# Kernel optimization log

Measured on AMD Instinct MI355X. Metric: run time of the kernel, lower is better.

## Reference

```python
import jax, jax.numpy as jnp
import numpy as np

B, S, D, F, E, DT, K = 4, 2048, 1024, 4096, 8, 256, 2


def setup_inputs() -> dict:
    key = jax.random.key(0)
    ks = jax.random.split(key, 8)
    scale_g = 1.0 / np.sqrt(D)
    scale_t = 1.0 / np.sqrt(DT)
    scale_1 = 1.0 / np.sqrt(D)
    scale_2 = 1.0 / np.sqrt(F)
    return {
        "inputs": jax.random.normal(ks[0], (B, S, D), dtype=jnp.float32),
        "task_param": jax.random.normal(ks[1], (B, 1, DT), dtype=jnp.float32),
        "Wg_in": jax.random.normal(ks[2], (D, E), dtype=jnp.float32) * scale_g,
        "bg_in": jnp.zeros((E,), dtype=jnp.float32),
        "Wg_task": jax.random.normal(ks[3], (DT, E), dtype=jnp.float32) * scale_t,
        "bg_task": jnp.zeros((E,), dtype=jnp.float32),
        "alpha": jnp.float32(0.5),
        "W1": jax.random.normal(ks[4], (E, D, F), dtype=jnp.float32) * scale_1,
        "b1": jnp.zeros((E, F), dtype=jnp.float32),
        "W2": jax.random.normal(ks[5], (E, F, D), dtype=jnp.float32) * scale_2,
        "b2": jnp.zeros((E, D), dtype=jnp.float32),
    }


def reference(inputs, task_param, Wg_in, bg_in, Wg_task, bg_task, alpha, W1, b1, W2, b2):
    # Gating: blend input-gate and task-gate logits ([B,1,E] broadcasts over S)
    input_logits = jnp.einsum('bsd,de->bse', inputs, Wg_in) + bg_in
    task_logits = jnp.einsum('btd,de->bte', task_param, Wg_task) + bg_task
    gate_logits = (1.0 - alpha) * input_logits + alpha * task_logits  # [B,S,E]

    topk_vals, selected = jax.lax.top_k(gate_logits, K)  # [B,S,K]

    # Load-balancing auxiliary loss (float32 softmax, as in the original)
    weights_softmax = jax.nn.softmax(gate_logits.astype(jnp.float32), axis=-1).astype(inputs.dtype)
    average_weight = jnp.mean(weights_softmax, axis=(0, 1))  # [E]
    onehot = jax.nn.one_hot(selected, E, dtype=inputs.dtype)  # [B,S,K,E]
    average_count = jnp.mean(onehot.sum(axis=2), axis=(0, 1))  # [E]
    l_aux = jnp.mean(average_weight * average_count) * E

    # Combine weights: softmax over the top-k gate values
    w = jax.nn.softmax(topk_vals.astype(jnp.float32), axis=-1).astype(inputs.dtype)  # [B,S,K]

    # Dense expert compute (same math as the per-expert gather/scatter loop)
    h = jax.nn.silu(jnp.einsum('bsd,edf->ebsf', inputs, W1) + b1[:, None, None, :])  # [E,B,S,F]
    expert_out = jnp.einsum('ebsf,efd->ebsd', h, W2) + b2[:, None, None, :]          # [E,B,S,D]

    picked = jnp.einsum('bske,ebsd->bskd', onehot, expert_out)  # [B,S,K,D]
    results = jnp.einsum('bsk,bskd->bsd', w, picked)            # [B,S,D]
    return results, l_aux.astype(jnp.float32)
```

## Files before the change

kernel.cpp:

```cpp
#include <hip/hip_runtime.h>

#define T_TOK 8192
#define D_DIM 1024
#define F_DIM 4096
#define E_EXP 8
#define DT_DIM 256
#define GBLK 256

#define A_XB   0u
#define A_WT   16777216u
#define A_H    83886080u
#define A_Y    226492416u
#define A_META 262144000u
#define MO_FILL   0
#define MO_PB     64
#define MO_NT     128
#define MO_PARTP  256
#define MO_PARTC  8448
#define MO_TILEE  16640
#define MO_TILERB 17664
#define MO_ROUTEE 18688
#define MO_ROUTEW 84224
#define MO_TSLOT  149760
#define MO_PTOK   215296
#define META_BYTES 284928
#define META_INTS  (META_BYTES/4)

using bf16x8 = __attribute__((ext_vector_type(8))) short;
using f32x4  = __attribute__((ext_vector_type(4))) float;
typedef unsigned short u16;

__device__ __forceinline__ u16 f2bf(float f) {
  union { float f; unsigned u; } v; v.f = f;
  unsigned r = v.u + 0x7FFFu + ((v.u >> 16) & 1u);
  return (u16)(r >> 16);
}
__device__ __forceinline__ float bf2f(u16 h) {
  union { unsigned u; float f; } v; v.u = ((unsigned)h) << 16; return v.f;
}
__device__ __forceinline__ void gload16(const void* gsrc, void* ldst) {
  __builtin_amdgcn_global_load_lds(
      (const __attribute__((address_space(1))) void*)gsrc,
      (__attribute__((address_space(3))) void*)ldst, 16, 0, 0);
}

__global__ void zerok(int* p, int n) {
  int i = blockIdx.x * 256 + threadIdx.x;
  if (i < n) p[i] = 0;
}

__global__ __launch_bounds__(256) void tcvt(const float* __restrict__ src,
                                            u16* __restrict__ dst, int R, int C) {
  __shared__ u16 tile[32][33];
  size_t off = (size_t)blockIdx.z * R * C;
  int cb = blockIdx.x * 32, rb = blockIdx.y * 32;
  int tx = threadIdx.x & 31, ty = threadIdx.x >> 5;
#pragma unroll
  for (int i = 0; i < 4; i++)
    tile[ty + i * 8][tx] = f2bf(src[off + (size_t)(rb + ty + i * 8) * C + cb + tx]);
  __syncthreads();
#pragma unroll
  for (int i = 0; i < 4; i++)
    dst[off + (size_t)(cb + ty + i * 8) * R + rb + tx] = tile[tx][ty + i * 8];
}

__global__ __launch_bounds__(256) void gating(
    const float* __restrict__ X, const float* __restrict__ TP,
    const float* __restrict__ Wg, const float* __restrict__ bg,
    const float* __restrict__ Wt, const float* __restrict__ bgt,
    const float* __restrict__ alphaP, u16* __restrict__ Xb, int* meta) {
  __shared__ float WgT[E_EXP * D_DIM];
  __shared__ float WtT[E_EXP * DT_DIM];
  __shared__ float wsP[4][8];
  __shared__ int   wsC[4][8];
  int tid = threadIdx.x;
  for (int i = tid; i < E_EXP * D_DIM; i += 256) { int d = i >> 3, e = i & 7; WgT[e * D_DIM + d] = Wg[i]; }
  for (int i = tid; i < E_EXP * DT_DIM; i += 256) { int d = i >> 3, e = i & 7; WtT[e * DT_DIM + d] = Wt[i]; }
  __syncthreads();
  int lane = tid & 63, wid = tid >> 6;
  int tb = blockIdx.x * 32;
  int b = tb >> 11;
  float alpha = alphaP[0];

  float tac[8] = {};
#pragma unroll
  for (int i = 0; i < 4; i++) {
    int d = lane + i * 64;
    float x = TP[b * DT_DIM + d];
#pragma unroll
    for (int e = 0; e < 8; e++) tac[e] += x * WtT[e * DT_DIM + d];
  }
  for (int off = 32; off > 0; off >>= 1)
#pragma unroll
    for (int e = 0; e < 8; e++) tac[e] += __shfl_xor(tac[e], off);
  float tl[8];
#pragma unroll
  for (int e = 0; e < 8; e++) tl[e] = alpha * (tac[e] + bgt[e]);

  float psum[8] = {};
  int   cnt[8] = {};
  for (int i = 0; i < 8; i++) {
    int t = tb + wid * 8 + i;
    const float* xr = X + (size_t)t * D_DIM;
    float acc[8] = {};
    u16 xb[16];
#pragma unroll 4
    for (int j = 0; j < 16; j++) {
      int d = lane + j * 64;
      float x = xr[d];
      xb[j] = f2bf(x);
#pragma unroll
      for (int e = 0; e < 8; e++) acc[e] += x * WgT[e * D_DIM + d];
    }
#pragma unroll
    for (int j = 0; j < 16; j++) Xb[(size_t)t * D_DIM + lane + j * 64] = xb[j];
    for (int off = 32; off > 0; off >>= 1)
#pragma unroll
      for (int e = 0; e < 8; e++) acc[e] += __shfl_xor(acc[e], off);
    float gl[8];
#pragma unroll
    for (int e = 0; e < 8; e++) gl[e] = (1.f - alpha) * (acc[e] + bg[e]) + tl[e];
    int e1 = 0;
#pragma unroll
    for (int e = 1; e < 8; e++) if (gl[e] > gl[e1]) e1 = e;
    int es = (e1 == 0) ? 1 : 0;
#pragma unroll
    for (int e = 0; e < 8; e++) if (e != e1 && gl[e] > gl[es]) es = e;
    float mx = gl[0];
#pragma unroll
    for (int e = 1; e < 8; e++) mx = fmaxf(mx, gl[e]);
    float pe[8], se = 0.f;
#pragma unroll
    for (int e = 0; e < 8; e++) { pe[e] = __expf(gl[e] - mx); se += pe[e]; }
    float inv = 1.f / se;
    if (lane == 0) {
#pragma unroll
      for (int e = 0; e < 8; e++) psum[e] += pe[e] * inv;
      cnt[e1]++; cnt[es]++;
      float w1 = 1.f / (1.f + __expf(gl[es] - gl[e1]));
      meta[MO_ROUTEE / 4 + 2 * t] = e1;
      meta[MO_ROUTEE / 4 + 2 * t + 1] = es;
      ((float*)meta)[MO_ROUTEW / 4 + 2 * t] = w1;
      ((float*)meta)[MO_ROUTEW / 4 + 2 * t + 1] = 1.f - w1;
    }
  }
  if (lane == 0) {
#pragma unroll
    for (int e = 0; e < 8; e++) { wsP[wid][e] = psum[e]; wsC[wid][e] = cnt[e]; }
  }
  __syncthreads();
  if (tid < 8) {
    float p = wsP[0][tid] + wsP[1][tid] + wsP[2][tid] + wsP[3][tid];
    int   c = wsC[0][tid] + wsC[1][tid] + wsC[2][tid] + wsC[3][tid];
    ((float*)meta)[MO_PARTP / 4 + blockIdx.x * 8 + tid] = p;
    meta[MO_PARTC / 4 + blockIdx.x * 8 + tid] = c;
  }
}

__global__ void plan(int* meta, float* out) {
  __shared__ float sp[8];
  __shared__ int   sc[8];
  int tid = threadIdx.x;
  if (blockIdx.x != 0) return;
  if (tid < 8) {
    const float* pp = (const float*)meta + MO_PARTP / 4;
    const int*   pc = meta + MO_PARTC / 4;
    float p = 0.f; int c = 0;
    for (int b = 0; b < GBLK; b++) { p += pp[b * 8 + tid]; c += pc[b * 8 + tid]; }
    sp[tid] = p; sc[tid] = c;
  }
  __syncthreads();
  if (tid == 0) {
    int* pb = meta + MO_PB / 4;
    int* tileE = meta + MO_TILEE / 4;
    int* tileRB = meta + MO_TILERB / 4;
    int base = 0, nt = 0;
    float la = 0.f;
    for (int e = 0; e < 8; e++) {
      int n = sc[e];
      pb[e] = base;
      int ntl = (n + 127) >> 7;
      for (int i = 0; i < ntl; i++) { tileE[nt] = e; tileRB[nt] = base + (i << 7); nt++; }
      base += ntl << 7;
      la += (sp[e] * (1.f / 8192.f)) * ((float)n * (1.f / 8192.f));
    }
    pb[8] = base;
    meta[MO_NT / 4] = nt;
    out[T_TOK * D_DIM] = la;
  }
}

__global__ __launch_bounds__(256) void fillk(int* meta) {
  int t = blockIdx.x * 256 + threadIdx.x;
  int lane = threadIdx.x & 63;
  int* pb = meta + MO_PB / 4;
  int* fl = meta + MO_FILL / 4;
  int* ptok = meta + MO_PTOK / 4;
  int* ts = meta + MO_TSLOT / 4;
  unsigned long long lmask = (1ull << lane) - 1;
#pragma unroll
  for (int k = 0; k < 2; k++) {
    int e = meta[MO_ROUTEE / 4 + 2 * t + k];
    int slot = 0;
    for (int ee = 0; ee < 8; ee++) {
      unsigned long long mask = __ballot(e == ee);
      if (e == ee) {
        int low = __ffsll((long long)mask) - 1;
        int pre = __popcll(mask & lmask);
        int base = 0;
        if (lane == low) base = atomicAdd(&fl[ee], __popcll(mask));
        base = __shfl(base, low);
        slot = pb[ee] + base + pre;
      }
    }
    ptok[slot] = t;
    ts[2 * t + k] = slot;
  }
}


__global__ __launch_bounds__(256) void gemm1(
    const u16* __restrict__ Xb, const u16* __restrict__ W1T,
    const float* __restrict__ b1, u16* __restrict__ H, const int* __restrict__ meta) {
  int nt = meta[MO_NT / 4];
  int bt = blockIdx.x;
  if (bt >= nt) return;
  int e = meta[MO_TILEE / 4 + bt];
  int rb = meta[MO_TILERB / 4 + bt];
  int cb = blockIdx.y * 128;
  const int* ptok = meta + MO_PTOK / 4;

  __shared__ short sA[128 * 64];
  __shared__ short sB[128 * 64];
  int tid = threadIdx.x, lane = tid & 63, wid = tid >> 6;
  int wr = wid >> 1, wc = wid & 1;

  int gsrc = ((lane & 7) ^ (lane >> 3)) * 8;
  const u16* srcA[4];
  const u16* srcB[4];
#pragma unroll
  for (int c = 0; c < 4; c++) {
    int rr = c * 32 + wid * 8 + (lane >> 3);
    int tok = ptok[rb + rr];
    srcA[c] = Xb + (size_t)tok * D_DIM + gsrc;
    srcB[c] = W1T + ((size_t)e * F_DIM + cb + rr) * D_DIM + gsrc;
  }

  f32x4 acc[4][4] = {};
  int g0 = lane >> 4, swz = lane & 7;
  int ra = wr * 64 + (lane & 15);
  int rn = wc * 64 + (lane & 15);
  for (int k0 = 0; k0 < D_DIM; k0 += 64) {
    __syncthreads();
#pragma unroll
    for (int c = 0; c < 4; c++) {
      gload16(srcA[c] + k0, (char*)sA + c * 4096 + wid * 1024);
      gload16(srcB[c] + k0, (char*)sB + c * 4096 + wid * 1024);
    }
    __syncthreads();
#pragma unroll
    for (int kk = 0; kk < 2; kk++) {
      bf16x8 af[4], bf[4];
      int gg = ((kk * 4 + g0) ^ swz) * 8;
#pragma unroll
      for (int m = 0; m < 4; m++)
        af[m] = *(const bf16x8*)(sA + (ra + m * 16) * 64 + gg);
#pragma unroll
      for (int n = 0; n < 4; n++)
        bf[n] = *(const bf16x8*)(sB + (rn + n * 16) * 64 + gg);
#pragma unroll
      for (int m = 0; m < 4; m++)
#pragma unroll
        for (int n = 0; n < 4; n++)
          acc[m][n] = __builtin_amdgcn_mfma_f32_16x16x32_bf16(af[m], bf[n], acc[m][n], 0, 0, 0);
    }
  }
  int rbase = wr * 64 + ((lane >> 4) << 2);
  int cbase = cb + wc * 64 + (lane & 15);
#pragma unroll
  for (int m = 0; m < 4; m++)
#pragma unroll
    for (int n = 0; n < 4; n++) {
      int f = cbase + n * 16;
      float bias = b1[e * F_DIM + f];
#pragma unroll
      for (int r = 0; r < 4; r++) {
        int p = rb + rbase + m * 16 + r;
        float v = acc[m][n][r] + bias;
        float s = v * (1.0f / (1.0f + __expf(-v)));
        H[(size_t)p * F_DIM + f] = f2bf(s);
      }
    }
}

__global__ __launch_bounds__(256) void gemm2(
    const u16* __restrict__ H, const u16* __restrict__ W2T,
    const float* __restrict__ b2, u16* __restrict__ Y, const int* __restrict__ meta) {
  int nt = meta[MO_NT / 4];
  int bt = blockIdx.y;
  if (bt >= nt) return;
  int e = meta[MO_TILEE / 4 + bt];
  int rb = meta[MO_TILERB / 4 + bt];
  int cb = blockIdx.x * 128;

  __shared__ short sA[128 * 64];
  __shared__ short sB[128 * 64];
  int tid = threadIdx.x, lane = tid & 63, wid = tid >> 6;
  int wr = wid >> 1, wc = wid & 1;

  int gsrc = ((lane & 7) ^ (lane >> 3)) * 8;
  const u16* srcA[4];
  const u16* srcB[4];
#pragma unroll
  for (int c = 0; c < 4; c++) {
    int rr = c * 32 + wid * 8 + (lane >> 3);
    srcA[c] = H + (size_t)(rb + rr) * F_DIM + gsrc;
    srcB[c] = W2T + ((size_t)e * D_DIM + cb + rr) * F_DIM + gsrc;
  }

  f32x4 acc[4][4] = {};
  int g0 = lane >> 4, swz = lane & 7;
  int ra = wr * 64 + (lane & 15);
  int rn = wc * 64 + (lane & 15);
  for (int k0 = 0; k0 < F_DIM; k0 += 64) {
    __syncthreads();
#pragma unroll
    for (int c = 0; c < 4; c++) {
      gload16(srcA[c] + k0, (char*)sA + c * 4096 + wid * 1024);
      gload16(srcB[c] + k0, (char*)sB + c * 4096 + wid * 1024);
    }
    __syncthreads();
#pragma unroll
    for (int kk = 0; kk < 2; kk++) {
      bf16x8 af[4], bf[4];
      int gg = ((kk * 4 + g0) ^ swz) * 8;
#pragma unroll
      for (int m = 0; m < 4; m++)
        af[m] = *(const bf16x8*)(sA + (ra + m * 16) * 64 + gg);
#pragma unroll
      for (int n = 0; n < 4; n++)
        bf[n] = *(const bf16x8*)(sB + (rn + n * 16) * 64 + gg);
#pragma unroll
      for (int m = 0; m < 4; m++)
#pragma unroll
        for (int n = 0; n < 4; n++)
          acc[m][n] = __builtin_amdgcn_mfma_f32_16x16x32_bf16(af[m], bf[n], acc[m][n], 0, 0, 0);
    }
  }
  int rbase = wr * 64 + ((lane >> 4) << 2);
  int cbase = cb + wc * 64 + (lane & 15);
#pragma unroll
  for (int m = 0; m < 4; m++)
#pragma unroll
    for (int n = 0; n < 4; n++) {
      int d = cbase + n * 16;
      float bias = b2[e * D_DIM + d];
#pragma unroll
      for (int r = 0; r < 4; r++) {
        int p = rb + rbase + m * 16 + r;
        Y[(size_t)p * D_DIM + d] = f2bf(acc[m][n][r] + bias);
      }
    }
}

__global__ __launch_bounds__(256) void combine(const u16* __restrict__ Y,
                                               const int* __restrict__ meta,
                                               float* __restrict__ out) {
  int t = blockIdx.x;
  const int* ts = meta + MO_TSLOT / 4;
  const float* rw = (const float*)meta + MO_ROUTEW / 4;
  int s1 = ts[2 * t], s2 = ts[2 * t + 1];
  float w1 = rw[2 * t], w2 = rw[2 * t + 1];
  int d0 = threadIdx.x * 4;
  ushort4 a = *(const ushort4*)(Y + (size_t)s1 * D_DIM + d0);
  ushort4 b = *(const ushort4*)(Y + (size_t)s2 * D_DIM + d0);
  float4 v;
  v.x = w1 * bf2f(a.x) + w2 * bf2f(b.x);
  v.y = w1 * bf2f(a.y) + w2 * bf2f(b.y);
  v.z = w1 * bf2f(a.z) + w2 * bf2f(b.z);
  v.w = w1 * bf2f(a.w) + w2 * bf2f(b.w);
  *(float4*)(out + (size_t)t * D_DIM + d0) = v;
}

extern "C" void kernel_launch(void* const* d_in, const int* in_sizes, int n_in,
                              void* d_out, int out_size, void* d_ws, size_t ws_size,
                              hipStream_t stream) {
  (void)in_sizes; (void)n_in; (void)out_size; (void)ws_size;
  const float* X    = (const float*)d_in[0];
  const float* TP   = (const float*)d_in[1];
  const float* Wg   = (const float*)d_in[2];
  const float* bg   = (const float*)d_in[3];
  const float* Wt   = (const float*)d_in[4];
  const float* bgt  = (const float*)d_in[5];
  const float* alp  = (const float*)d_in[6];
  const float* W1   = (const float*)d_in[7];
  const float* b1   = (const float*)d_in[8];
  const float* W2   = (const float*)d_in[9];
  const float* b2   = (const float*)d_in[10];
  float* out = (float*)d_out;
  char* ws = (char*)d_ws;
  u16* Xb = (u16*)(ws + A_XB);
  u16* WT = (u16*)(ws + A_WT);
  u16* H  = (u16*)(ws + A_H);
  u16* Y  = (u16*)(ws + A_Y);
  int* meta = (int*)(ws + A_META);

  zerok<<<(META_INTS + 255) / 256, 256, 0, stream>>>(meta, META_INTS);
  tcvt<<<dim3(F_DIM / 32, D_DIM / 32, E_EXP), 256, 0, stream>>>(W1, WT, D_DIM, F_DIM);
  gating<<<GBLK, 256, 0, stream>>>(X, TP, Wg, bg, Wt, bgt, alp, Xb, meta);
  plan<<<1, 64, 0, stream>>>(meta, out);
  fillk<<<T_TOK / 256, 256, 0, stream>>>(meta);
  gemm1<<<dim3(136, F_DIM / 128), 256, 0, stream>>>(Xb, WT, b1, H, meta);
  tcvt<<<dim3(D_DIM / 32, F_DIM / 32, E_EXP), 256, 0, stream>>>(W2, WT, F_DIM, D_DIM);
  gemm2<<<dim3(8, 136), 256, 0, stream>>>(H, WT, b2, Y, meta);
  combine<<<T_TOK, 256, 0, stream>>>(Y, meta, out);
}
```

Baseline: 660.3 us.

## Double-buffer LDS tiles in expert GEMMs and remap blocks for XCD locality

Both grouped GEMMs now use two LDS buffers and prefetch the next K-slice with async global-to-LDS loads while MFMAs run on the current one. Partial vmcnt waits and raised wave priority during compute replace the two syncthreads per step. The grid is flattened to 1D, with a remap that spreads consecutive block ids across the 8 XCDs so blocks sharing a tile land together and reuse L2. LDS use per block doubles to 64 KB, with launch bounds requesting 2 blocks per CU.

After: 664.6 us. No clear change (+0.7%).

```diff
diff --git a/kernel.cpp b/kernel.cpp
--- a/kernel.cpp
+++ b/kernel.cpp
@@ -219,19 +219,21 @@
 }
 
 
-__global__ __launch_bounds__(256) void gemm1(
+__global__ __launch_bounds__(256, 2) void gemm1(
     const u16* __restrict__ Xb, const u16* __restrict__ W1T,
     const float* __restrict__ b1, u16* __restrict__ H, const int* __restrict__ meta) {
+  int id = blockIdx.x;
+  int wg = (id & 7) * 544 + (id >> 3);
+  int bt = wg % 136;
+  int cb = (wg / 136) * 128;
   int nt = meta[MO_NT / 4];
-  int bt = blockIdx.x;
   if (bt >= nt) return;
   int e = meta[MO_TILEE / 4 + bt];
   int rb = meta[MO_TILERB / 4 + bt];
-  int cb = blockIdx.y * 128;
   const int* ptok = meta + MO_PTOK / 4;
 
-  __shared__ short sA[128 * 64];
-  __shared__ short sB[128 * 64];
+  __shared__ short sA[2][128 * 64];
+  __shared__ short sB[2][128 * 64];
   int tid = threadIdx.x, lane = tid & 63, wid = tid >> 6;
   int wr = wid >> 1, wc = wid & 1;
 
@@ -250,30 +252,45 @@
   int g0 = lane >> 4, swz = lane & 7;
   int ra = wr * 64 + (lane & 15);
   int rn = wc * 64 + (lane & 15);
+
+#define STAGE1(buf, k0)                                                  \
+  _Pragma("unroll") for (int c = 0; c < 4; c++) {                        \
+    gload16(srcA[c] + (k0), (char*)&sA[buf][0] + c * 4096 + wid * 1024); \
+    gload16(srcB[c] + (k0), (char*)&sB[buf][0] + c * 4096 + wid * 1024); \
+  }
+
+  STAGE1(0, 0);
+  int cur = 0;
   for (int k0 = 0; k0 < D_DIM; k0 += 64) {
-    __syncthreads();
-#pragma unroll
-    for (int c = 0; c < 4; c++) {
-      gload16(srcA[c] + k0, (char*)sA + c * 4096 + wid * 1024);
-      gload16(srcB[c] + k0, (char*)sB + c * 4096 + wid * 1024);
-    }
-    __syncthreads();
+    if (k0 + 64 < D_DIM) {
+      STAGE1(cur ^ 1, k0 + 64);
+      asm volatile("s_waitcnt vmcnt(8)" ::: "memory");
+    } else {
+      asm volatile("s_waitcnt vmcnt(0)" ::: "memory");
+    }
+    __builtin_amdgcn_s_barrier();
+    __builtin_amdgcn_s_setprio(1);
+    const short* pA = &sA[cur][0];
+    const short* pB = &sB[cur][0];
 #pragma unroll
     for (int kk = 0; kk < 2; kk++) {
       bf16x8 af[4], bf[4];
       int gg = ((kk * 4 + g0) ^ swz) * 8;
 #pragma unroll
       for (int m = 0; m < 4; m++)
-        af[m] = *(const bf16x8*)(sA + (ra + m * 16) * 64 + gg);
+        af[m] = *(const bf16x8*)(pA + (ra + m * 16) * 64 + gg);
 #pragma unroll
       for (int n = 0; n < 4; n++)
-        bf[n] = *(const bf16x8*)(sB + (rn + n * 16) * 64 + gg);
+        bf[n] = *(const bf16x8*)(pB + (rn + n * 16) * 64 + gg);
 #pragma unroll
       for (int m = 0; m < 4; m++)
 #pragma unroll
         for (int n = 0; n < 4; n++)
           acc[m][n] = __builtin_amdgcn_mfma_f32_16x16x32_bf16(af[m], bf[n], acc[m][n], 0, 0, 0);
     }
+    __builtin_amdgcn_s_setprio(0);
+    __builtin_amdgcn_s_barrier();
+    cur ^= 1;
   }
   int rbase = wr * 64 + ((lane >> 4) << 2);
   int cbase = cb + wc * 64 + (lane & 15);
@@ -293,18 +310,20 @@
     }
 }
 
-__global__ __launch_bounds__(256) void gemm2(
+__global__ __launch_bounds__(256, 2) void gemm2(
     const u16* __restrict__ H, const u16* __restrict__ W2T,
     const float* __restrict__ b2, u16* __restrict__ Y, const int* __restrict__ meta) {
+  int id = blockIdx.x;
+  int wg = (id & 7) * 136 + (id >> 3);
+  int bt = wg >> 3;
+  int cb = (wg & 7) * 128;
   int nt = meta[MO_NT / 4];
-  int bt = blockIdx.y;
   if (bt >= nt) return;
   int e = meta[MO_TILEE / 4 + bt];
   int rb = meta[MO_TILERB / 4 + bt];
-  int cb = blockIdx.x * 128;
-
-  __shared__ short sA[128 * 64];
-  __shared__ short sB[128 * 64];
+
+  __shared__ short sA[2][128 * 64];
+  __shared__ short sB[2][128 * 64];
   int tid = threadIdx.x, lane = tid & 63, wid = tid >> 6;
   int wr = wid >> 1, wc = wid & 1;
 
@@ -322,30 +341,45 @@
   int g0 = lane >> 4, swz = lane & 7;
   int ra = wr * 64 + (lane & 15);
   int rn = wc * 64 + (lane & 15);
+
+#define STAGE2(buf, k0)                                                  \
+  _Pragma("unroll") for (int c = 0; c < 4; c++) {                        \
+    gload16(srcA[c] + (k0), (char*)&sA[buf][0] + c * 4096 + wid * 1024); \
+    gload16(srcB[c] + (k0), (char*)&sB[buf][0] + c * 4096 + wid * 1024); \
+  }
+
+  STAGE2(0, 0);
+  int cur = 0;
   for (int k0 = 0; k0 < F_DIM; k0 += 64) {
-    __syncthreads();
-#pragma unroll
-    for (int c = 0; c < 4; c++) {
-      gload16(srcA[c] + k0, (char*)sA + c * 4096 + wid * 1024);
-      gload16(srcB[c] + k0, (char*)sB + c * 4096 + wid * 1024);
-    }
-    __syncthreads();
+    if (k0 + 64 < F_DIM) {
+      STAGE2(cur ^ 1, k0 + 64);
+      asm volatile("s_waitcnt vmcnt(8)" ::: "memory");
+    } else {
+      asm volatile("s_waitcnt vmcnt(0)" ::: "memory");
+    }
+    __builtin_amdgcn_s_barrier();
+    __builtin_amdgcn_s_setprio(1);
+    const short* pA = &sA[cur][0];
+    const short* pB = &sB[cur][0];
 #pragma unroll
     for (int kk = 0; kk < 2; kk++) {
       bf16x8 af[4], bf[4];
       int gg = ((kk * 4 + g0) ^ swz) * 8;
 #pragma unroll
       for (int m = 0; m < 4; m++)
-        af[m] = *(const bf16x8*)(sA + (ra + m * 16) * 64 + gg);
+        af[m] = *(const bf16x8*)(pA + (ra + m * 16) * 64 + gg);
 #pragma unroll
       for (int n = 0; n < 4; n++)
-        bf[n] = *(const bf16x8*)(sB + (rn + n * 16) * 64 + gg);
+        bf[n] = *(const bf16x8*)(pB + (rn + n * 16) * 64 + gg);
 #pragma unroll
       for (int m = 0; m < 4; m++)
 #pragma unroll
         for (int n = 0; n < 4; n++)
           acc[m][n] = __builtin_amdgcn_mfma_f32_16x16x32_bf16(af[m], bf[n], acc[m][n], 0, 0, 0);
     }
+    __builtin_amdgcn_s_setprio(0);
+    __builtin_amdgcn_s_barrier();
+    cur ^= 1;
   }
   int rbase = wr * 64 + ((lane >> 4) << 2);
   int cbase = cb + wc * 64 + (lane & 15);
@@ -410,8 +444,8 @@
   gating<<<GBLK, 256, 0, stream>>>(X, TP, Wg, bg, Wt, bgt, alp, Xb, meta);
   plan<<<1, 64, 0, stream>>>(meta, out);
   fillk<<<T_TOK / 256, 256, 0, stream>>>(meta);
-  gemm1<<<dim3(136, F_DIM / 128), 256, 0, stream>>>(Xb, WT, b1, H, meta);
+  gemm1<<<4352, 256, 0, stream>>>(Xb, WT, b1, H, meta);
   tcvt<<<dim3(D_DIM / 32, F_DIM / 32, E_EXP), 256, 0, stream>>>(W2, WT, F_DIM, D_DIM);
-  gemm2<<<dim3(8, 136), 256, 0, stream>>>(H, WT, b2, Y, meta);
+  gemm2<<<1088, 256, 0, stream>>>(H, WT, b2, Y, meta);
   combine<<<T_TOK, 256, 0, stream>>>(Y, meta, out);
 }
```

## Enlarge grouped GEMM tiles to 256x256 with double-buffered LDS pipeline

Applied to the files above, without the earlier changes.

Both expert GEMMs move from 128x128 tiles with 256 threads to 256x256 tiles with 512 threads. Global-to-LDS loads are double-buffered so the next K-slice is fetched while the current one runs on MFMA. The block index is remapped for XCD-aware scheduling, the routing plan now emits 256-row tiles over 128-padded segments, and stores are guarded by a per-expert row end. Larger tiles raise arithmetic intensity and cut redundant weight traffic, but the last tile of each expert wastes more work and register and LDS pressure goes up.

New measurement: 740.1 us. +12.1%, slower.

```diff
diff --git a/kernel.cpp b/kernel.cpp
--- a/kernel.cpp
+++ b/kernel.cpp
@@ -179,9 +179,10 @@
     for (int e = 0; e < 8; e++) {
       int n = sc[e];
       pb[e] = base;
-      int ntl = (n + 127) >> 7;
-      for (int i = 0; i < ntl; i++) { tileE[nt] = e; tileRB[nt] = base + (i << 7); nt++; }
-      base += ntl << 7;
+      int seg = ((n + 127) >> 7) << 7;
+      int ntl = (seg + 255) >> 8;
+      for (int i = 0; i < ntl; i++) { tileE[nt] = e; tileRB[nt] = base + (i << 8); nt++; }
+      base += seg;
       la += (sp[e] * (1.f / 8192.f)) * ((float)n * (1.f / 8192.f));
     }
     pb[8] = base;
@@ -219,146 +220,135 @@
 }
 
 
-__global__ __launch_bounds__(256) void gemm1(
+#define GEMM_PRE(KDIM)                                                        \
+  __shared__ short sA[2][256 * 64];                                           \
+  __shared__ short sB[2][256 * 64];                                           \
+  int tid = threadIdx.x, lane = tid & 63, wid = tid >> 6;                     \
+  int wr = wid >> 2, wc = wid & 3;                                            \
+  int sw8 = ((tid & 7) ^ ((tid >> 3) & 7)) * 8;                               \
+  int dstb = tid * 16;                                                        \
+  f32x4 acc[8][4] = {};                                                       \
+  int rA = wr * 128 + (lane & 15);                                            \
+  int rB = wc * 64 + (lane & 15);                                             \
+  int gx = lane & 7, gb = lane >> 4;
+
+#define GEMM_STAGE(buf, kt)                                                   \
+  _Pragma("unroll") for (int l = 0; l < 4; l++) {                             \
+    gload16(srcA[l] + (size_t)(kt) * 64, (char*)&sA[buf][0] + l * 8192 + dstb); \
+    gload16(srcB[l] + (size_t)(kt) * 64, (char*)&sB[buf][0] + l * 8192 + dstb); \
+  }
+
+#define GEMM_LOOP(NK)                                                         \
+  GEMM_STAGE(0, 0)                                                            \
+  for (int kt = 0; kt < (NK); kt++) {                                         \
+    int c = kt & 1;                                                           \
+    asm volatile("s_waitcnt vmcnt(0)" ::: "memory");                          \
+    __builtin_amdgcn_s_barrier();                                             \
+    if (kt + 1 < (NK)) { GEMM_STAGE(c ^ 1, kt + 1) }                          \
+    const short* pA = &sA[c][0];                                              \
+    const short* pB = &sB[c][0];                                              \
+    bf16x8 bfr[4][2];                                                         \
+    _Pragma("unroll") for (int n = 0; n < 4; n++)                             \
+      _Pragma("unroll") for (int kk = 0; kk < 2; kk++)                        \
+        bfr[n][kk] = *(const bf16x8*)(pB + (rB + n * 16) * 64 + (((kk * 4 + gb) ^ gx) * 8)); \
+    __builtin_amdgcn_s_setprio(1);                                            \
+    _Pragma("unroll") for (int m = 0; m < 8; m++) {                           \
+      bf16x8 a0 = *(const bf16x8*)(pA + (rA + m * 16) * 64 + (((gb) ^ gx) * 8));       \
+      bf16x8 a1 = *(const bf16x8*)(pA + (rA + m * 16) * 64 + (((4 + gb) ^ gx) * 8));   \
+      _Pragma("unroll") for (int n = 0; n < 4; n++) {                         \
+        acc[m][n] = __builtin_amdgcn_mfma_f32_16x16x32_bf16(a0, bfr[n][0], acc[m][n], 0, 0, 0); \
+        acc[m][n] = __builtin_amdgcn_mfma_f32_16x16x32_bf16(a1, bfr[n][1], acc[m][n], 0, 0, 0); \
+      }                                                                       \
+    }                                                                         \
+    __builtin_amdgcn_s_setprio(0);                                            \
+  }
+
+__global__ __launch_bounds__(512, 2) void gemm1(
     const u16* __restrict__ Xb, const u16* __restrict__ W1T,
     const float* __restrict__ b1, u16* __restrict__ H, const int* __restrict__ meta) {
+  int id = blockIdx.x;
+  int wg = (id & 7) * 144 + (id >> 3);
+  int bt = wg >> 4, cbi = wg & 15;
   int nt = meta[MO_NT / 4];
-  int bt = blockIdx.x;
   if (bt >= nt) return;
   int e = meta[MO_TILEE / 4 + bt];
   int rb = meta[MO_TILERB / 4 + bt];
-  int cb = blockIdx.y * 128;
+  int rowEnd = meta[MO_PB / 4 + e + 1];
+  int cb = cbi * 256;
   const int* ptok = meta + MO_PTOK / 4;
 
-  __shared__ short sA[128 * 64];
-  __shared__ short sB[128 * 64];
-  int tid = threadIdx.x, lane = tid & 63, wid = tid >> 6;
-  int wr = wid >> 1, wc = wid & 1;
-
-  int gsrc = ((lane & 7) ^ (lane >> 3)) * 8;
+  GEMM_PRE(D_DIM)
   const u16* srcA[4];
   const u16* srcB[4];
 #pragma unroll
-  for (int c = 0; c < 4; c++) {
-    int rr = c * 32 + wid * 8 + (lane >> 3);
-    int tok = ptok[rb + rr];
-    srcA[c] = Xb + (size_t)tok * D_DIM + gsrc;
-    srcB[c] = W1T + ((size_t)e * F_DIM + cb + rr) * D_DIM + gsrc;
-  }
-
-  f32x4 acc[4][4] = {};
-  int g0 = lane >> 4, swz = lane & 7;
-  int ra = wr * 64 + (lane & 15);
-  int rn = wc * 64 + (lane & 15);
-  for (int k0 = 0; k0 < D_DIM; k0 += 64) {
-    __syncthreads();
-#pragma unroll
-    for (int c = 0; c < 4; c++) {
-      gload16(srcA[c] + k0, (char*)sA + c * 4096 + wid * 1024);
-      gload16(srcB[c] + k0, (char*)sB + c * 4096 + wid * 1024);
-    }
-    __syncthreads();
-#pragma unroll
-    for (int kk = 0; kk < 2; kk++) {
-      bf16x8 af[4], bf[4];
-      int gg = ((kk * 4 + g0) ^ swz) * 8;
-#pragma unroll
-      for (int m = 0; m < 4; m++)
-        af[m] = *(const bf16x8*)(sA + (ra + m * 16) * 64 + gg);
-#pragma unroll
-      for (int n = 0; n < 4; n++)
-        bf[n] = *(const bf16x8*)(sB + (rn + n * 16) * 64 + gg);
-#pragma unroll
-      for (int m = 0; m < 4; m++)
-#pragma unroll
-        for (int n = 0; n < 4; n++)
-          acc[m][n] = __builtin_amdgcn_mfma_f32_16x16x32_bf16(af[m], bf[n], acc[m][n], 0, 0, 0);
-    }
-  }
-  int rbase = wr * 64 + ((lane >> 4) << 2);
+  for (int l = 0; l < 4; l++) {
+    int r = l * 64 + (tid >> 3);
+    int ri = rb + r; ri = ri < 17407 ? ri : 17407;
+    int tok = ptok[ri];
+    srcA[l] = Xb + (size_t)tok * D_DIM + sw8;
+    srcB[l] = W1T + ((size_t)e * F_DIM + cb + r) * D_DIM + sw8;
+  }
+
+  GEMM_LOOP(16)
+
+  int rbase = rb + wr * 128 + ((lane >> 4) << 2);
   int cbase = cb + wc * 64 + (lane & 15);
 #pragma unroll
-  for (int m = 0; m < 4; m++)
+  for (int m = 0; m < 8; m++)
 #pragma unroll
     for (int n = 0; n < 4; n++) {
       int f = cbase + n * 16;
       float bias = b1[e * F_DIM + f];
 #pragma unroll
       for (int r = 0; r < 4; r++) {
-        int p = rb + rbase + m * 16 + r;
-        float v = acc[m][n][r] + bias;
-        float s = v * (1.0f / (1.0f + __expf(-v)));
-        H[(size_t)p * F_DIM + f] = f2bf(s);
+        int p = rbase + m * 16 + r;
+        if (p < rowEnd) {
+          float v = acc[m][n][r] + bias;
+          float s = v * (1.0f / (1.0f + __expf(-v)));
+          H[(size_t)p * F_DIM + f] = f2bf(s);
+        }
       }
     }
 }
 
-__global__ __launch_bounds__(256) void gemm2(
+__global__ __launch_bounds__(512, 2) void gemm2(
     const u16* __restrict__ H, const u16* __restrict__ W2T,
     const float* __restrict__ b2, u16* __restrict__ Y, const int* __restrict__ meta) {
+  int id = blockIdx.x;
+  int wg = (id & 7) * 36 + (id >> 3);
+  int bt = wg >> 2, cbi = wg & 3;
   int nt = meta[MO_NT / 4];
-  int bt = blockIdx.y;
   if (bt >= nt) return;
   int e = meta[MO_TILEE / 4 + bt];
   int rb = meta[MO_TILERB / 4 + bt];
-  int cb = blockIdx.x * 128;
-
-  __shared__ short sA[128 * 64];
-  __shared__ short sB[128 * 64];
-  int tid = threadIdx.x, lane = tid & 63, wid = tid >> 6;
-  int wr = wid >> 1, wc = wid & 1;
-
-  int gsrc = ((lane & 7) ^ (lane >> 3)) * 8;
+  int rowEnd = meta[MO_PB / 4 + e + 1];
+  int cb = cbi * 256;
+
+  GEMM_PRE(F_DIM)
   const u16* srcA[4];
   const u16* srcB[4];
 #pragma unroll
-  for (int c = 0; c < 4; c++) {
-    int rr = c * 32 + wid * 8 + (lane >> 3);
-    srcA[c] = H + (size_t)(rb + rr) * F_DIM + gsrc;
-    srcB[c] = W2T + ((size_t)e * D_DIM + cb + rr) * F_DIM + gsrc;
-  }
-
-  f32x4 acc[4][4] = {};
-  int g0 = lane >> 4, swz = lane & 7;
-  int ra = wr * 64 + (lane & 15);
-  int rn = wc * 64 + (lane & 15);
-  for (int k0 = 0; k0 < F_DIM; k0 += 64) {
-    __syncthreads();
-#pragma unroll
-    for (int c = 0; c < 4; c++) {
-      gload16(srcA[c] + k0, (char*)sA + c * 4096 + wid * 1024);
-      gload16(srcB[c] + k0, (char*)sB + c * 4096 + wid * 1024);
-    }
-    __syncthreads();
-#pragma unroll
-    for (int kk = 0; kk < 2; kk++) {
-      bf16x8 af[4], bf[4];
-      int gg = ((kk * 4 + g0) ^ swz) * 8;
-#pragma unroll
-      for (int m = 0; m < 4; m++)
-        af[m] = *(const bf16x8*)(sA + (ra + m * 16) * 64 + gg);
-#pragma unroll
-      for (int n = 0; n < 4; n++)
-        bf[n] = *(const bf16x8*)(sB + (rn + n * 16) * 64 + gg);
-#pragma unroll
-      for (int m = 0; m < 4; m++)
-#pragma unroll
-        for (int n = 0; n < 4; n++)
-          acc[m][n] = __builtin_amdgcn_mfma_f32_16x16x32_bf16(af[m], bf[n], acc[m][n], 0, 0, 0);
-    }
-  }
-  int rbase = wr * 64 + ((lane >> 4) << 2);
+  for (int l = 0; l < 4; l++) {
+    int r = l * 64 + (tid >> 3);
+    srcA[l] = H + (size_t)(rb + r) * F_DIM + sw8;
+    srcB[l] = W2T + ((size_t)e * D_DIM + cb + r) * F_DIM + sw8;
+  }
+
+  GEMM_LOOP(64)
+
+  int rbase = rb + wr * 128 + ((lane >> 4) << 2);
   int cbase = cb + wc * 64 + (lane & 15);
 #pragma unroll
-  for (int m = 0; m < 4; m++)
+  for (int m = 0; m < 8; m++)
 #pragma unroll
     for (int n = 0; n < 4; n++) {
       int d = cbase + n * 16;
       float bias = b2[e * D_DIM + d];
 #pragma unroll
       for (int r = 0; r < 4; r++) {
-        int p = rb + rbase + m * 16 + r;
-        Y[(size_t)p * D_DIM + d] = f2bf(acc[m][n][r] + bias);
+        int p = rbase + m * 16 + r;
+        if (p < rowEnd)
+          Y[(size_t)p * D_DIM + d] = f2bf(acc[m][n][r] + bias);
       }
     }
 }
@@ -410,8 +400,8 @@
   gating<<<GBLK, 256, 0, stream>>>(X, TP, Wg, bg, Wt, bgt, alp, Xb, meta);
   plan<<<1, 64, 0, stream>>>(meta, out);
   fillk<<<T_TOK / 256, 256, 0, stream>>>(meta);
-  gemm1<<<dim3(136, F_DIM / 128), 256, 0, stream>>>(Xb, WT, b1, H, meta);
+  gemm1<<<1152, 512, 0, stream>>>(Xb, WT, b1, H, meta);
   tcvt<<<dim3(D_DIM / 32, F_DIM / 32, E_EXP), 256, 0, stream>>>(W2, WT, F_DIM, D_DIM);
-  gemm2<<<dim3(8, 136), 256, 0, stream>>>(H, WT, b2, Y, meta);
+  gemm2<<<288, 512, 0, stream>>>(H, WT, b2, Y, meta);
   combine<<<T_TOK, 256, 0, stream>>>(Y, meta, out);
 }
```
